# Kernel optimization log

Hardware: AMD Instinct MI355X
Metric: run time of the kernel (lower is better)

The kernel has to match this reference:

```python
import jax, jax.numpy as jnp
import numpy as np

D_MODEL = 1024
NHEAD = 16
D_HEAD = D_MODEL // NHEAD
DIM_FF = 4096
EPS = 1e-5

def layer_norm(x, scale, bias):
    mu = jnp.mean(x, axis=-1, keepdims=True)
    var = jnp.mean(jnp.square(x - mu), axis=-1, keepdims=True)
    return (x - mu) * jax.lax.rsqrt(var + EPS) * scale + bias

def setup_inputs() -> dict:
    key = jax.random.key(0)
    ks = jax.random.split(key, 8)
    B, T, D = 4, 2048, D_MODEL
    s = 1.0 / np.sqrt(D)
    sf = 1.0 / np.sqrt(DIM_FF)
    return {
        "x": jax.random.normal(ks[0], (B, T, D), dtype=jnp.float32),
        "ln1_scale": jnp.ones((D,), jnp.float32),
        "ln1_bias": jnp.zeros((D,), jnp.float32),
        "qkv_w": jax.random.normal(ks[1], (3 * D, D), jnp.float32) * s,  # torch Linear weight [out,in]
        "out_w": jax.random.normal(ks[2], (D, D), jnp.float32) * s,
        "ln2_scale": jnp.ones((D,), jnp.float32),
        "ln2_bias": jnp.zeros((D,), jnp.float32),
        "fc1_w": jax.random.normal(ks[3], (DIM_FF, D), jnp.float32) * s,
        "fc1_b": jnp.zeros((DIM_FF,), jnp.float32),
        "fc2_w": jax.random.normal(ks[4], (D, DIM_FF), jnp.float32) * sf,
        "fc2_b": jnp.zeros((D,), jnp.float32),
    }

def reference(x, ln1_scale, ln1_bias, qkv_w, out_w, ln2_scale, ln2_bias, fc1_w, fc1_b, fc2_w, fc2_b):
    B, T, D = x.shape
    # --- attention sublayer (pre-LN) ---
    h = layer_norm(x, ln1_scale, ln1_bias)
    qkv = jnp.einsum('btd,ed->bte', h, qkv_w)  # [B,T,3D]
    q, k, v = jnp.split(qkv, 3, axis=-1)
    def heads(t):
        return t.reshape(B, T, NHEAD, D_HEAD).transpose(0, 2, 1, 3)  # [B,H,T,dh]
    q, k, v = heads(q), heads(k), heads(v)
    scores = jnp.einsum('bhqd,bhkd->bhqk', q, k) / np.sqrt(D_HEAD)
    attn = jax.nn.softmax(scores, axis=-1)
    o = jnp.einsum('bhqk,bhkd->bhqd', attn, v)
    o = o.transpose(0, 2, 1, 3).reshape(B, T, D)
    h = jnp.einsum('btd,ed->bte', o, out_w)
    x = x + h
    # --- FFN sublayer (pre-LN) ---
    h = layer_norm(x, ln2_scale, ln2_bias)
    h = jnp.einsum('btd,fd->btf', h, fc1_w) + fc1_b
    h = jax.nn.gelu(h, approximate=False)
    h = jnp.einsum('btf,df->btd', h, fc2_w) + fc2_b
    return x + h
```

## Files before the change

### kernel.cpp

```cpp
#include <hip/hip_runtime.h>
#include <hip/hip_bf16.h>
#include <math.h>

typedef unsigned short u16;
typedef unsigned int u32;
typedef short s8v __attribute__((ext_vector_type(8)));
typedef float f4v __attribute__((ext_vector_type(4)));

#define D_MODEL 1024
#define DIMFF   4096
#define SEQ     2048
#define TOKENS  8192

#define QSCALE 0.18033688011112042f

static __device__ __forceinline__ u16 f2bf(float f) {
    unsigned int u = __builtin_bit_cast(unsigned int, f);
    unsigned int lsb = (u >> 16) & 1u;
    u += 0x7fffu + lsb;
    return (u16)(u >> 16);
}

static __device__ __forceinline__ void gl2lds16(const u16* g, u16* l) {
    __builtin_amdgcn_global_load_lds(
        (__attribute__((address_space(1))) void*)(void*)g,
        (__attribute__((address_space(3))) void*)l, 16, 0, 0);
}

__global__ __launch_bounds__(256) void cvt_kernel(const float* __restrict__ in,
                                                  u16* __restrict__ out, int n4) {
    int i = blockIdx.x * 256 + threadIdx.x;
    if (i < n4) {
        float4 v = ((const float4*)in)[i];
        ushort4 o;
        o.x = f2bf(v.x); o.y = f2bf(v.y); o.z = f2bf(v.z); o.w = f2bf(v.w);
        ((ushort4*)out)[i] = o;
    }
}

__global__ __launch_bounds__(256) void ln_kernel(const float* __restrict__ x,
                                                 const float* __restrict__ scale,
                                                 const float* __restrict__ bias,
                                                 u16* __restrict__ out) {
    int row = blockIdx.x;
    int t = threadIdx.x;
    const float* xr = x + (size_t)row * D_MODEL;
    float4 v = ((const float4*)xr)[t];
    float s  = v.x + v.y + v.z + v.w;
    float ss = v.x*v.x + v.y*v.y + v.z*v.z + v.w*v.w;
    #pragma unroll
    for (int off = 1; off < 64; off <<= 1) {
        s  += __shfl_xor(s, off);
        ss += __shfl_xor(ss, off);
    }
    __shared__ float red[8];
    int wave = t >> 6, lane = t & 63;
    if (lane == 0) { red[wave] = s; red[4 + wave] = ss; }
    __syncthreads();
    float S  = red[0] + red[1] + red[2] + red[3];
    float SS = red[4] + red[5] + red[6] + red[7];
    float mu  = S * (1.0f / D_MODEL);
    float var = SS * (1.0f / D_MODEL) - mu * mu;
    float r = rsqrtf(var + 1e-5f);
    float4 sc = ((const float4*)scale)[t];
    float4 bi = ((const float4*)bias)[t];
    ushort4 o;
    o.x = f2bf((v.x - mu) * r * sc.x + bi.x);
    o.y = f2bf((v.y - mu) * r * sc.y + bi.y);
    o.z = f2bf((v.z - mu) * r * sc.z + bi.z);
    o.w = f2bf((v.w - mu) * r * sc.w + bi.w);
    ((ushort4*)(out + (size_t)row * D_MODEL))[t] = o;
}

#define BM 128
#define BN 128
#define BK 64

template<int MODE>
__global__ __launch_bounds__(256) void gemm_kernel(
        const u16* __restrict__ A, const u16* __restrict__ W,
        const float* __restrict__ bias, const float* __restrict__ res,
        void* __restrict__ outp, void* __restrict__ out2, int M, int N, int K) {
    __shared__ __attribute__((aligned(16))) u16 As[BM * BK];
    __shared__ __attribute__((aligned(16))) u16 Bs[BN * BK];
    int t = threadIdx.x;
    int lane = t & 63, w = t >> 6;
    int nb = N / BN;
    int bm = blockIdx.x / nb, bn = blockIdx.x % nb;
    int m0 = bm * BM, n0 = bn * BN;
    int wm = (w >> 1) * 64, wn = (w & 1) * 64;
    int lr = lane >> 4, lc = lane & 15, sw = lc & 7;

    f4v acc[4][4] = {};

    int arow[4], acg[4];
    #pragma unroll
    for (int n = 0; n < 4; ++n) {
        int chunk = (w * 4 + n) * 64 + lane;
        arow[n] = chunk >> 3;
        acg[n]  = ((chunk & 7) ^ (arow[n] & 7)) * 8;
    }

    for (int k0 = 0; k0 < K; k0 += BK) {
        #pragma unroll
        for (int n = 0; n < 4; ++n) {
            gl2lds16(&A[(size_t)(m0 + arow[n]) * K + k0 + acg[n]], &As[(w * 4 + n) * 512]);
            gl2lds16(&W[(size_t)(n0 + arow[n]) * K + k0 + acg[n]], &Bs[(w * 4 + n) * 512]);
        }
        __syncthreads();
        #pragma unroll
        for (int ks = 0; ks < 2; ++ks) {
            s8v af[4], bfr[4];
            #pragma unroll
            for (int i = 0; i < 4; ++i)
                af[i] = *(const s8v*)&As[(wm + i * 16 + lc) * BK + ((ks * 4 + lr) ^ sw) * 8];
            #pragma unroll
            for (int j = 0; j < 4; ++j)
                bfr[j] = *(const s8v*)&Bs[(wn + j * 16 + lc) * BK + ((ks * 4 + lr) ^ sw) * 8];
            #pragma unroll
            for (int i = 0; i < 4; ++i)
                #pragma unroll
                for (int j = 0; j < 4; ++j)
                    acc[i][j] = __builtin_amdgcn_mfma_f32_16x16x32_bf16(af[i], bfr[j], acc[i][j], 0, 0, 0);
        }
        __syncthreads();
    }

    #pragma unroll
    for (int i = 0; i < 4; ++i) {
        #pragma unroll
        for (int j = 0; j < 4; ++j) {
            int col = n0 + wn + j * 16 + lc;
            float b = (MODE == 2 || MODE == 3) ? bias[col] : 0.f;
            if (MODE == 4) {
                int colbase = n0 + wn + j * 16;
                if (colbase < 2048) {
                    float sc = (colbase < 1024) ? QSCALE : 1.0f;
                    #pragma unroll
                    for (int r = 0; r < 4; ++r) {
                        int row = m0 + wm + i * 16 + lr * 4 + r;
                        ((u16*)outp)[(size_t)row * 2048 + col] = f2bf(acc[i][j][r] * sc);
                    }
                } else {
                    int dlin = col - 2048;
                    int h = dlin >> 6, dd = dlin & 63;
                    int trow = m0 + wm + i * 16 + lr * 4;
                    int bb = trow >> 11, tt = trow & 2047;
                    int bh = bb * 16 + h;
                    ushort4 vv;
                    vv.x = f2bf(acc[i][j][0]); vv.y = f2bf(acc[i][j][1]);
                    vv.z = f2bf(acc[i][j][2]); vv.w = f2bf(acc[i][j][3]);
                    *(ushort4*)&((u16*)out2)[((size_t)bh * 64 + dd) * SEQ + tt] = vv;
                }
            } else {
                #pragma unroll
                for (int r = 0; r < 4; ++r) {
                    int row = m0 + wm + i * 16 + lr * 4 + r;
                    size_t idx = (size_t)row * N + col;
                    float v = acc[i][j][r];
                    if (MODE == 0) {
                        ((u16*)outp)[idx] = f2bf(v);
                    } else if (MODE == 1) {
                        ((float*)outp)[idx] = res[idx] + v;
                    } else if (MODE == 2) {
                        float z = v + b;
                        float g = 0.5f * z * (1.0f + erff(z * 0.70710678118654752f));
                        ((u16*)outp)[idx] = f2bf(g);
                    } else {
                        ((float*)outp)[idx] = res[idx] + v + b;
                    }
                }
            }
        }
    }
}

__global__ __launch_bounds__(256) void attn_kernel(const u16* __restrict__ qk,
                                                   const u16* __restrict__ vt,
                                                   u16* __restrict__ out) {
    __shared__ __attribute__((aligned(16))) u16 Ks[64 * 64];
    __shared__ __attribute__((aligned(16))) u16 Vts[64 * 64];
    __shared__ __attribute__((aligned(16))) u16 Ps[64 * 72];
    int t = threadIdx.x, lane = t & 63, w = t >> 6;
    int blk = blockIdx.x;
    int bh = blk >> 5, qt = blk & 31;
    int b = bh >> 4, h = bh & 15;
    size_t tok0 = (size_t)b * SEQ;
    int q0 = qt * 64;
    int lr = lane >> 4, lc = lane & 15, sw = lc & 7;

    s8v aq[2];
    {
        const u16* qp = qk + (tok0 + q0 + w * 16 + lc) * 2048 + h * 64;
        aq[0] = *(const s8v*)(qp + lr * 8);
        aq[1] = *(const s8v*)(qp + 32 + lr * 8);
    }
    f4v o[4] = {};
    float lp = 0.f;

    int srow[2], scg[2];
    #pragma unroll
    for (int n = 0; n < 2; ++n) {
        int chunk = (w * 2 + n) * 64 + lane;
        srow[n] = chunk >> 3;
        scg[n]  = ((chunk & 7) ^ (srow[n] & 7)) * 8;
    }
    const u16* vbase = vt + (size_t)bh * 64 * SEQ;

    for (int kt = 0; kt < SEQ / 64; ++kt) {
        #pragma unroll
        for (int n = 0; n < 2; ++n) {
            gl2lds16(&qk[(tok0 + kt * 64 + srow[n]) * 2048 + 1024 + h * 64 + scg[n]],
                     &Ks[(w * 2 + n) * 512]);
            gl2lds16(&vbase[(size_t)srow[n] * SEQ + kt * 64 + scg[n]],
                     &Vts[(w * 2 + n) * 512]);
        }
        __syncthreads();

        f4v s[4] = {};
        #pragma unroll
        for (int j = 0; j < 4; ++j)
            #pragma unroll
            for (int kc = 0; kc < 2; ++kc) {
                s8v bk = *(const s8v*)&Ks[(j * 16 + lc) * 64 + ((kc * 4 + lr) ^ sw) * 8];
                s[j] = __builtin_amdgcn_mfma_f32_16x16x32_bf16(bk, aq[kc], s[j], 0, 0, 0);
            }

        #pragma unroll
        for (int j = 0; j < 4; ++j) {
            u32 ib[4];
            #pragma unroll
            for (int r = 0; r < 4; ++r) {
                ib[r] = (u32)fmaf(s[j][r], 8388608.0f, 1064992506.0f);
                lp += __builtin_bit_cast(float, ib[r]);
            }
            uint2 pk;
            pk.x = __builtin_amdgcn_perm(ib[1], ib[0], 0x07060302);
            pk.y = __builtin_amdgcn_perm(ib[3], ib[2], 0x07060302);
            *(uint2*)&Ps[(w * 16 + lc) * 72 + j * 16 + lr * 4] = pk;
        }

        s8v ap[2];
        ap[0] = *(const s8v*)&Ps[(w * 16 + lc) * 72 + lr * 8];
        ap[1] = *(const s8v*)&Ps[(w * 16 + lc) * 72 + 32 + lr * 8];
        #pragma unroll
        for (int j = 0; j < 4; ++j)
            #pragma unroll
            for (int kc = 0; kc < 2; ++kc) {
                s8v bv = *(const s8v*)&Vts[(j * 16 + lc) * 64 + ((kc * 4 + lr) ^ sw) * 8];
                o[j] = __builtin_amdgcn_mfma_f32_16x16x32_bf16(ap[kc], bv, o[j], 0, 0, 0);
            }
        __syncthreads();
    }

    lp += __shfl_xor(lp, 16);
    lp += __shfl_xor(lp, 32);
    float linv[4];
    #pragma unroll
    for (int r = 0; r < 4; ++r) linv[r] = 1.0f / __shfl(lp, lr * 4 + r);
    #pragma unroll
    for (int j = 0; j < 4; ++j)
        #pragma unroll
        for (int r = 0; r < 4; ++r) {
            size_t row = tok0 + q0 + w * 16 + lr * 4 + r;
            out[row * 1024 + h * 64 + j * 16 + lc] = f2bf(o[j][r] * linv[r]);
        }
}

extern "C" void kernel_launch(void* const* d_in, const int* in_sizes, int n_in,
                              void* d_out, int out_size, void* d_ws, size_t ws_size,
                              hipStream_t stream) {
    const float* x      = (const float*)d_in[0];
    const float* ln1_s  = (const float*)d_in[1];
    const float* ln1_b  = (const float*)d_in[2];
    const float* qkv_w  = (const float*)d_in[3];
    const float* out_w  = (const float*)d_in[4];
    const float* ln2_s  = (const float*)d_in[5];
    const float* ln2_b  = (const float*)d_in[6];
    const float* fc1_w  = (const float*)d_in[7];
    const float* fc1_b  = (const float*)d_in[8];
    const float* fc2_w  = (const float*)d_in[9];
    const float* fc2_b  = (const float*)d_in[10];
    float* out = (float*)d_out;

    char* ws = (char*)d_ws;
    size_t off = 0;
    auto alloc = [&](size_t bytes) -> void* {
        void* p = ws + off;
        off += (bytes + 255) & ~(size_t)255;
        return p;
    };
    u16* wq  = (u16*)alloc((size_t)3072 * 1024 * 2);
    u16* wo  = (u16*)alloc((size_t)1024 * 1024 * 2);
    u16* w1  = (u16*)alloc((size_t)4096 * 1024 * 2);
    u16* w2  = (u16*)alloc((size_t)1024 * 4096 * 2);
    u16* h1  = (u16*)alloc((size_t)TOKENS * 1024 * 2);
    u16* qk  = (u16*)alloc((size_t)TOKENS * 2048 * 2);
    float* x2 = (float*)alloc((size_t)TOKENS * 1024 * 4);
    u16* g   = (u16*)alloc((size_t)TOKENS * 4096 * 2);
    u16* attn_out = h1;
    u16* h2       = qk;
    u16* vt       = (u16*)x2;

    cvt_kernel<<<(3072 * 1024 / 4 + 255) / 256, 256, 0, stream>>>(qkv_w, wq, 3072 * 1024 / 4);
    cvt_kernel<<<(1024 * 1024 / 4 + 255) / 256, 256, 0, stream>>>(out_w, wo, 1024 * 1024 / 4);
    cvt_kernel<<<(4096 * 1024 / 4 + 255) / 256, 256, 0, stream>>>(fc1_w, w1, 4096 * 1024 / 4);
    cvt_kernel<<<(1024 * 4096 / 4 + 255) / 256, 256, 0, stream>>>(fc2_w, w2, 1024 * 4096 / 4);

    ln_kernel<<<TOKENS, 256, 0, stream>>>(x, ln1_s, ln1_b, h1);
    gemm_kernel<4><<<(TOKENS / BM) * (3072 / BN), 256, 0, stream>>>(
        h1, wq, nullptr, nullptr, qk, vt, TOKENS, 3072, 1024);
    attn_kernel<<<64 * 32, 256, 0, stream>>>(qk, vt, attn_out);
    gemm_kernel<1><<<(TOKENS / BM) * (1024 / BN), 256, 0, stream>>>(
        attn_out, wo, nullptr, x, x2, nullptr, TOKENS, 1024, 1024);
    ln_kernel<<<TOKENS, 256, 0, stream>>>(x2, ln2_s, ln2_b, h2);
    gemm_kernel<2><<<(TOKENS / BM) * (DIMFF / BN), 256, 0, stream>>>(
        h2, w1, fc1_b, nullptr, g, nullptr, TOKENS, DIMFF, 1024);
    gemm_kernel<3><<<(TOKENS / BM) * (1024 / BN), 256, 0, stream>>>(
        g, w2, fc2_b, x2, out, nullptr, TOKENS, 1024, DIMFF);
}
```

Before: 546.8 us.

## Switch attention to 32x32x16 MFMA with 128-row query tiles and merge weight casts

The attention kernel now uses 32x32x16 bf16 MFMA instructions. Each block covers 128 query rows instead of 64, which halves the number of blocks and doubles the reuse of each loaded K/V tile. The P tile is staged in LDS with a 68-element row stride, and the row sums go through shared memory for the final normalisation. The four weight-conversion launches are merged into one kernel writing contiguous buffers, and an unused epilogue mode is dropped. The risks are more register pressure and fewer blocks for occupancy.

```diff
diff --git a/kernel.cpp b/kernel.cpp
--- a/kernel.cpp
+++ b/kernel.cpp
@@ -6,6 +6,8 @@
 typedef unsigned int u32;
 typedef short s8v __attribute__((ext_vector_type(8)));
 typedef float f4v __attribute__((ext_vector_type(4)));
+typedef float f16v __attribute__((ext_vector_type(16)));
+typedef u32 u4v __attribute__((ext_vector_type(4)));
 
 #define D_MODEL 1024
 #define DIMFF   4096
@@ -27,15 +29,24 @@
         (__attribute__((address_space(3))) void*)l, 16, 0, 0);
 }
 
-__global__ __launch_bounds__(256) void cvt_kernel(const float* __restrict__ in,
-                                                  u16* __restrict__ out, int n4) {
+#define N4_QKV  786432
+#define N4_WO   262144
+#define N4_FC   1048576
+__global__ __launch_bounds__(256) void cvt_all_kernel(const float* __restrict__ s0,
+                                                      const float* __restrict__ s1,
+                                                      const float* __restrict__ s2,
+                                                      const float* __restrict__ s3,
+                                                      u16* __restrict__ dst) {
     int i = blockIdx.x * 256 + threadIdx.x;
-    if (i < n4) {
-        float4 v = ((const float4*)in)[i];
-        ushort4 o;
-        o.x = f2bf(v.x); o.y = f2bf(v.y); o.z = f2bf(v.z); o.w = f2bf(v.w);
-        ((ushort4*)out)[i] = o;
-    }
+    const float* src; int j;
+    if (i < N4_QKV)                    { src = s0; j = i; }
+    else if (i < N4_QKV + N4_WO)       { src = s1; j = i - N4_QKV; }
+    else if (i < N4_QKV + N4_WO + N4_FC) { src = s2; j = i - N4_QKV - N4_WO; }
+    else                               { src = s3; j = i - N4_QKV - N4_WO - N4_FC; }
+    float4 v = ((const float4*)src)[j];
+    ushort4 o;
+    o.x = f2bf(v.x); o.y = f2bf(v.y); o.z = f2bf(v.z); o.w = f2bf(v.w);
+    ((ushort4*)dst)[i] = o;
 }
 
 __global__ __launch_bounds__(256) void ln_kernel(const float* __restrict__ x,
@@ -158,9 +169,7 @@
                     int row = m0 + wm + i * 16 + lr * 4 + r;
                     size_t idx = (size_t)row * N + col;
                     float v = acc[i][j][r];
-                    if (MODE == 0) {
-                        ((u16*)outp)[idx] = f2bf(v);
-                    } else if (MODE == 1) {
+                    if (MODE == 1) {
                         ((float*)outp)[idx] = res[idx] + v;
                     } else if (MODE == 2) {
                         float z = v + b;
@@ -180,22 +189,23 @@
                                                    u16* __restrict__ out) {
     __shared__ __attribute__((aligned(16))) u16 Ks[64 * 64];
     __shared__ __attribute__((aligned(16))) u16 Vts[64 * 64];
-    __shared__ __attribute__((aligned(16))) u16 Ps[64 * 72];
+    __shared__ __attribute__((aligned(16))) u16 Ps[128 * 68];
+    __shared__ float l_s[128];
     int t = threadIdx.x, lane = t & 63, w = t >> 6;
+    int l31 = lane & 31, hi = lane >> 5;
     int blk = blockIdx.x;
-    int bh = blk >> 5, qt = blk & 31;
+    int bh = blk >> 4, qt = blk & 15;
     int b = bh >> 4, h = bh & 15;
     size_t tok0 = (size_t)b * SEQ;
-    int q0 = qt * 64;
-    int lr = lane >> 4, lc = lane & 15, sw = lc & 7;
-
-    s8v aq[2];
+    int q0 = qt * 128;
+
+    s8v bq[4];
     {
-        const u16* qp = qk + (tok0 + q0 + w * 16 + lc) * 2048 + h * 64;
-        aq[0] = *(const s8v*)(qp + lr * 8);
-        aq[1] = *(const s8v*)(qp + 32 + lr * 8);
-    }
-    f4v o[4] = {};
+        const u16* qp = qk + (tok0 + q0 + w * 32 + l31) * 2048 + h * 64 + hi * 8;
+        #pragma unroll
+        for (int dch = 0; dch < 4; ++dch) bq[dch] = *(const s8v*)(qp + dch * 16);
+    }
+    f16v o[2] = {};
     float lp = 0.f;
 
     int srow[2], scg[2];
@@ -206,6 +216,7 @@
         scg[n]  = ((chunk & 7) ^ (srow[n] & 7)) * 8;
     }
     const u16* vbase = vt + (size_t)bh * 64 * SEQ;
+    int prow = (w * 32 + l31) * 68;
 
     for (int kt = 0; kt < SEQ / 64; ++kt) {
         #pragma unroll
@@ -217,54 +228,57 @@
         }
         __syncthreads();
 
-        f4v s[4] = {};
-        #pragma unroll
-        for (int j = 0; j < 4; ++j)
-            #pragma unroll
-            for (int kc = 0; kc < 2; ++kc) {
-                s8v bk = *(const s8v*)&Ks[(j * 16 + lc) * 64 + ((kc * 4 + lr) ^ sw) * 8];
-                s[j] = __builtin_amdgcn_mfma_f32_16x16x32_bf16(bk, aq[kc], s[j], 0, 0, 0);
+        f16v s_[2] = {};
+        #pragma unroll
+        for (int kb = 0; kb < 2; ++kb)
+            #pragma unroll
+            for (int dch = 0; dch < 4; ++dch) {
+                s8v ak = *(const s8v*)&Ks[(kb * 32 + l31) * 64 + ((dch * 2 + hi) ^ (l31 & 7)) * 8];
+                s_[kb] = __builtin_amdgcn_mfma_f32_32x32x16_bf16(ak, bq[dch], s_[kb], 0, 0, 0);
             }
 
         #pragma unroll
-        for (int j = 0; j < 4; ++j) {
-            u32 ib[4];
-            #pragma unroll
-            for (int r = 0; r < 4; ++r) {
-                ib[r] = (u32)fmaf(s[j][r], 8388608.0f, 1064992506.0f);
-                lp += __builtin_bit_cast(float, ib[r]);
+        for (int kb = 0; kb < 2; ++kb)
+            #pragma unroll
+            for (int g = 0; g < 4; ++g) {
+                u32 ib[4];
+                #pragma unroll
+                for (int rr = 0; rr < 4; ++rr) {
+                    ib[rr] = (u32)fmaf(s_[kb][g * 4 + rr], 8388608.0f, 1064992506.0f);
+                    lp += __builtin_bit_cast(float, ib[rr]);
+                }
+                uint2 pk;
+                pk.x = __builtin_amdgcn_perm(ib[1], ib[0], 0x07060302);
+                pk.y = __builtin_amdgcn_perm(ib[3], ib[2], 0x07060302);
+                *(uint2*)&Ps[prow + kb * 32 + g * 8 + hi * 4] = pk;
             }
-            uint2 pk;
-            pk.x = __builtin_amdgcn_perm(ib[1], ib[0], 0x07060302);
-            pk.y = __builtin_amdgcn_perm(ib[3], ib[2], 0x07060302);
-            *(uint2*)&Ps[(w * 16 + lc) * 72 + j * 16 + lr * 4] = pk;
-        }
-
-        s8v ap[2];
-        ap[0] = *(const s8v*)&Ps[(w * 16 + lc) * 72 + lr * 8];
-        ap[1] = *(const s8v*)&Ps[(w * 16 + lc) * 72 + 32 + lr * 8];
-        #pragma unroll
-        for (int j = 0; j < 4; ++j)
-            #pragma unroll
-            for (int kc = 0; kc < 2; ++kc) {
-                s8v bv = *(const s8v*)&Vts[(j * 16 + lc) * 64 + ((kc * 4 + lr) ^ sw) * 8];
-                o[j] = __builtin_amdgcn_mfma_f32_16x16x32_bf16(ap[kc], bv, o[j], 0, 0, 0);
+
+        #pragma unroll
+        for (int ch = 0; ch < 4; ++ch) {
+            uint2 u0 = *(const uint2*)&Ps[prow + ch * 16 + hi * 8];
+            uint2 u1 = *(const uint2*)&Ps[prow + ch * 16 + hi * 8 + 4];
+            u4v tmp; tmp.x = u0.x; tmp.y = u0.y; tmp.z = u1.x; tmp.w = u1.y;
+            s8v ap = __builtin_bit_cast(s8v, tmp);
+            #pragma unroll
+            for (int dblk = 0; dblk < 2; ++dblk) {
+                s8v bv = *(const s8v*)&Vts[(dblk * 32 + l31) * 64 + ((ch * 2 + hi) ^ (l31 & 7)) * 8];
+                o[dblk] = __builtin_amdgcn_mfma_f32_32x32x16_bf16(ap, bv, o[dblk], 0, 0, 0);
             }
+        }
         __syncthreads();
     }
 
-    lp += __shfl_xor(lp, 16);
     lp += __shfl_xor(lp, 32);
-    float linv[4];
-    #pragma unroll
-    for (int r = 0; r < 4; ++r) linv[r] = 1.0f / __shfl(lp, lr * 4 + r);
-    #pragma unroll
-    for (int j = 0; j < 4; ++j)
-        #pragma unroll
-        for (int r = 0; r < 4; ++r) {
-            size_t row = tok0 + q0 + w * 16 + lr * 4 + r;
-            out[row * 1024 + h * 64 + j * 16 + lc] = f2bf(o[j][r] * linv[r]);
-        }
+    l_s[w * 32 + l31] = 1.0f / lp;
+    #pragma unroll
+    for (int r = 0; r < 16; ++r) {
+        int qrl = (r & 3) + 8 * (r >> 2) + 4 * hi;
+        float linv = l_s[w * 32 + qrl];
+        size_t row = tok0 + q0 + w * 32 + qrl;
+        #pragma unroll
+        for (int dblk = 0; dblk < 2; ++dblk)
+            out[row * 1024 + h * 64 + dblk * 32 + l31] = f2bf(o[dblk][r] * linv);
+    }
 }
 
 extern "C" void kernel_launch(void* const* d_in, const int* in_sizes, int n_in,
@@ -301,16 +315,15 @@
     u16* attn_out = h1;
     u16* h2       = qk;
     u16* vt       = (u16*)x2;
-
-    cvt_kernel<<<(3072 * 1024 / 4 + 255) / 256, 256, 0, stream>>>(qkv_w, wq, 3072 * 1024 / 4);
-    cvt_kernel<<<(1024 * 1024 / 4 + 255) / 256, 256, 0, stream>>>(out_w, wo, 1024 * 1024 / 4);
-    cvt_kernel<<<(4096 * 1024 / 4 + 255) / 256, 256, 0, stream>>>(fc1_w, w1, 4096 * 1024 / 4);
-    cvt_kernel<<<(1024 * 4096 / 4 + 255) / 256, 256, 0, stream>>>(fc2_w, w2, 1024 * 4096 / 4);
+    (void)wo; (void)w1; (void)w2;
+
+    cvt_all_kernel<<<(N4_QKV + N4_WO + 2 * N4_FC) / 256, 256, 0, stream>>>(
+        qkv_w, out_w, fc1_w, fc2_w, wq);
 
     ln_kernel<<<TOKENS, 256, 0, stream>>>(x, ln1_s, ln1_b, h1);
     gemm_kernel<4><<<(TOKENS / BM) * (3072 / BN), 256, 0, stream>>>(
         h1, wq, nullptr, nullptr, qk, vt, TOKENS, 3072, 1024);
-    attn_kernel<<<64 * 32, 256, 0, stream>>>(qk, vt, attn_out);
+    attn_kernel<<<64 * 16, 256, 0, stream>>>(qk, vt, attn_out);
     gemm_kernel<1><<<(TOKENS / BM) * (1024 / BN), 256, 0, stream>>>(
         attn_out, wo, nullptr, x, x2, nullptr, TOKENS, 1024, 1024);
     ln_kernel<<<TOKENS, 256, 0, stream>>>(x2, ln2_s, ln2_b, h2);
```

Measured after the change: 539.0 us. No clear change (-1.4%).
